# Kernel tuning notes

Measured on AMD Instinct MI355X. Metric: run time of the kernel, lower is better.

The kernel has to match this reference:

```python
import jax, jax.numpy as jnp
import numpy as np

B, S, H = 64, 2048, 1024
X0, X1, X2, A = 1024, 512, 512, 512


def setup_inputs() -> dict:
    key = jax.random.key(0)
    ks = jax.random.split(key, 11)
    wb = np.sqrt(6.0 / (H + A)).astype(np.float32)
    w0b = np.sqrt(6.0 / (X0 + A)).astype(np.float32)
    w1b = np.sqrt(6.0 / (X1 + A)).astype(np.float32)
    w2b = np.sqrt(6.0 / (X2 + A)).astype(np.float32)
    return {
        "hidden_states": jax.random.normal(ks[0], (B, S, H), dtype=jnp.float32),
        "x0_hidden_states": jax.random.normal(ks[1], (B, X0), dtype=jnp.float32),
        "x1_hidden_states": jax.random.normal(ks[2], (B, X1), dtype=jnp.float32),
        "x2_hidden_states": jax.random.normal(ks[3], (B, X2), dtype=jnp.float32),
        "lengths": jax.random.randint(ks[4], (B,), 1, S + 1),
        # torch Linear stores weight as [out, in]
        "Wh_w": jax.random.uniform(ks[5], (A, H), minval=-wb, maxval=wb, dtype=jnp.float32),
        "Wh_b": jnp.zeros((A,), dtype=jnp.float32),
        "W0_w": jax.random.uniform(ks[6], (A, X0), minval=-w0b, maxval=w0b, dtype=jnp.float32),
        "W1_w": jax.random.uniform(ks[7], (A, X1), minval=-w1b, maxval=w1b, dtype=jnp.float32),
        "W2_w": jax.random.uniform(ks[8], (A, X2), minval=-w2b, maxval=w2b, dtype=jnp.float32),
        "V_w": 0.1 * jax.random.normal(ks[9], (1, A), dtype=jnp.float32),
    }


def reference(hidden_states, x0_hidden_states, x1_hidden_states, x2_hidden_states,
              lengths, Wh_w, Wh_b, W0_w, W1_w, W2_w, V_w):
    # Ah: [B,S,A]; context projections broadcast over seq dim
    Ah = jnp.einsum('bsh,ah->bsa', hidden_states, Wh_w) + Wh_b
    A0 = (x0_hidden_states @ W0_w.T)[:, None, :]
    A1 = (x1_hidden_states @ W1_w.T)[:, None, :]
    A2 = (x2_hidden_states @ W2_w.T)[:, None, :]
    w = jax.nn.relu(Ah + A0 + A1 + A2)
    scores = jnp.einsum('bsa,a->bs', w, V_w[0])  # [B,S]
    mask = jnp.arange(scores.shape[1])[None, :] < lengths[:, None]
    scores = jnp.where(mask, scores, -jnp.inf)
    attention_prob = jax.nn.softmax(scores, axis=1)
    output = jnp.einsum('bs,bsh->bh', attention_prob, hidden_states)
    return output, attention_prob
```

## Files before the change

kernel.cpp:

```cpp
#include <hip/hip_runtime.h>
#include <hip/hip_bf16.h>
#include <stdint.h>

#define B_ 64
#define S_ 2048
#define H_ 1024
#define X0_ 1024
#define X1_ 512
#define X2_ 512
#define A_ 512

typedef __attribute__((ext_vector_type(8))) short short8;
typedef __attribute__((ext_vector_type(8))) __bf16 bf16x8;
typedef __attribute__((ext_vector_type(4))) float floatx4;

typedef __attribute__((address_space(1))) const void glb_cv;
typedef __attribute__((address_space(3))) void lds_v;

__device__ inline unsigned short f2bf(float f) {
    union { float f; unsigned u; } v; v.f = f;
    unsigned u = v.u;
    unsigned r = u + 0x7FFF + ((u >> 16) & 1);
    return (unsigned short)(r >> 16);
}

__device__ inline short hwbf(float f) {
    return (short)__builtin_bit_cast(unsigned short, __float2bfloat16(f));
}

__global__ void k_convert_wh(const float* __restrict__ wh, unsigned short* __restrict__ whb) {
    int i = (blockIdx.x * 256 + threadIdx.x) * 4;
    float4 f = *(const float4*)(wh + i);
    ushort4 o;
    o.x = f2bf(f.x); o.y = f2bf(f.y); o.z = f2bf(f.z); o.w = f2bf(f.w);
    *(ushort4*)(whb + i) = o;
}

__global__ void k_ctx(const float* __restrict__ x0, const float* __restrict__ x1,
                      const float* __restrict__ x2, const float* __restrict__ w0,
                      const float* __restrict__ w1, const float* __restrict__ w2,
                      const float* __restrict__ bias, float* __restrict__ ctx) {
    __shared__ float xs[X0_ + X1_ + X2_];
    int b = blockIdx.x >> 4;
    int a0 = (blockIdx.x & 15) << 5;
    int t = threadIdx.x;
    for (int i = t; i < X0_; i += 256) xs[i] = x0[b * X0_ + i];
    for (int i = t; i < X1_; i += 256) xs[X0_ + i] = x1[b * X1_ + i];
    for (int i = t; i < X2_; i += 256) xs[X0_ + X1_ + i] = x2[b * X2_ + i];
    __syncthreads();
    int wave = t >> 6, lane = t & 63;
    for (int j = 0; j < 8; j++) {
        int a = a0 + wave * 8 + j;
        float acc = 0.f;
        const float* r0 = w0 + (size_t)a * X0_;
        for (int k = lane; k < X0_; k += 64) acc += r0[k] * xs[k];
        const float* r1 = w1 + (size_t)a * X1_;
        for (int k = lane; k < X1_; k += 64) acc += r1[k] * xs[X0_ + k];
        const float* r2 = w2 + (size_t)a * X2_;
        for (int k = lane; k < X2_; k += 64) acc += r2[k] * xs[X0_ + X1_ + k];
        for (int off = 32; off; off >>= 1) acc += __shfl_down(acc, off, 64);
        if (lane == 0) ctx[b * A_ + a] = acc + bias[a];
    }
}

__launch_bounds__(256, 2)
__global__ void k_scores(const float* __restrict__ hidden, const unsigned short* __restrict__ whb,
                         const float* __restrict__ ctx, const float* __restrict__ vw,
                         const int* __restrict__ lengths, float* __restrict__ partial) {
    int g = blockIdx.x;
    int xcd = g & 7;
    int i4 = g >> 3;
    int nblk = i4 & 3;
    int grp = xcd * 128 + (i4 >> 2);
    int b = grp >> 4;
    int mt = grp & 15;
    int s0 = mt * 128;
    if (s0 >= lengths[b]) return;
    int n0b = nblk * 128;

    __shared__ unsigned short As[128 * 32];
    __shared__ unsigned short Bs[128 * 32];
    __shared__ float sred[4][64];

    int t = threadIdx.x;
    int wv = t >> 6, lane = t & 63;
    int nl = lane & 15, quad = lane >> 4;
    int wm0 = (wv & 1) * 64;
    int wn0 = (wv >> 1) * 64;

    int c0 = wv * 64 + lane;
    int c1 = c0 + 256;
    const float* abase = hidden + (size_t)(b * S_ + s0) * H_;
    const unsigned short* bbase = whb + (size_t)n0b * H_;
    size_t aoff0 = (size_t)(c0 >> 2) * H_ + (c0 & 3) * 8;
    size_t aoff1 = (size_t)(c1 >> 2) * H_ + (c1 & 3) * 8;

    float4 a0a = *(const float4*)(abase + aoff0);
    float4 a0b = *(const float4*)(abase + aoff0 + 4);
    float4 a1a = *(const float4*)(abase + aoff1);
    float4 a1b = *(const float4*)(abase + aoff1 + 4);

    floatx4 acc[4][4];
#pragma unroll
    for (int i = 0; i < 4; i++)
#pragma unroll
        for (int j = 0; j < 4; j++) acc[i][j] = (floatx4){0.f, 0.f, 0.f, 0.f};

    for (int k0 = 0; k0 < H_; k0 += 32) {
#pragma unroll
        for (int i = 0; i < 2; i++) {
            int c = wv * 64 + i * 256 + lane;
            const unsigned short* gb = bbase + (size_t)(c >> 2) * H_ + k0 + (c & 3) * 8;
            __builtin_amdgcn_global_load_lds((glb_cv*)gb,
                (lds_v*)(Bs + (wv * 64 + i * 256) * 8), 16, 0, 0);
        }
        short8 pa, pb;
        pa[0] = hwbf(a0a.x); pa[1] = hwbf(a0a.y); pa[2] = hwbf(a0a.z); pa[3] = hwbf(a0a.w);
        pa[4] = hwbf(a0b.x); pa[5] = hwbf(a0b.y); pa[6] = hwbf(a0b.z); pa[7] = hwbf(a0b.w);
        pb[0] = hwbf(a1a.x); pb[1] = hwbf(a1a.y); pb[2] = hwbf(a1a.z); pb[3] = hwbf(a1a.w);
        pb[4] = hwbf(a1b.x); pb[5] = hwbf(a1b.y); pb[6] = hwbf(a1b.z); pb[7] = hwbf(a1b.w);
        *(short8*)&As[c0 * 8] = pa;
        *(short8*)&As[c1 * 8] = pb;
        __syncthreads();

        if (k0 + 32 < H_) {
            a0a = *(const float4*)(abase + aoff0 + k0 + 32);
            a0b = *(const float4*)(abase + aoff0 + k0 + 36);
            a1a = *(const float4*)(abase + aoff1 + k0 + 32);
            a1b = *(const float4*)(abase + aoff1 + k0 + 36);
        }

        short8 af[4];
#pragma unroll
        for (int m = 0; m < 4; m++)
            af[m] = *(const short8*)&As[(wm0 + m * 16 + nl) * 32 + quad * 8];
#pragma unroll
        for (int n = 0; n < 4; n++) {
            short8 bfr = *(const short8*)&Bs[(wn0 + n * 16 + nl) * 32 + quad * 8];
            bf16x8 bfv = __builtin_bit_cast(bf16x8, bfr);
#pragma unroll
            for (int m = 0; m < 4; m++) {
                bf16x8 afv = __builtin_bit_cast(bf16x8, af[m]);
                acc[m][n] = __builtin_amdgcn_mfma_f32_16x16x32_bf16(afv, bfv, acc[m][n], 0, 0, 0);
            }
        }
        __syncthreads();
    }

    float cv[4], cc[4];
#pragma unroll
    for (int n = 0; n < 4; n++) {
        int gn = n0b + wn0 + n * 16 + nl;
        cv[n] = vw[gn];
        cc[n] = ctx[b * A_ + gn];
    }
#pragma unroll
    for (int m = 0; m < 4; m++) {
#pragma unroll
        for (int r = 0; r < 4; r++) {
            float sv = 0.f;
#pragma unroll
            for (int n = 0; n < 4; n++) {
                float x = acc[m][n][r] + cc[n];
                sv += (x > 0.f) ? x * cv[n] : 0.f;
            }
#pragma unroll
            for (int off = 1; off < 16; off <<= 1) sv += __shfl_xor(sv, off, 16);
            if (nl == 0) sred[wv][m * 16 + quad * 4 + r] = sv;
        }
    }
    __syncthreads();
    if (t < 128) {
        int h = t >> 6;
        float s = sred[h][t & 63] + sred[h + 2][t & 63];
        partial[((size_t)nblk * B_ + b) * S_ + s0 + t] = s;
    }
}

__global__ void k_softmax(const float* __restrict__ partial, const int* __restrict__ lengths,
                          float* __restrict__ scores, float* __restrict__ probs) {
    int b = blockIdx.x;
    int len = lengths[b];
    int t = threadIdx.x;
    __shared__ float red[256];
    float mx = -1e30f;
    for (int s = t; s < len; s += 256) {
        float sc = partial[(size_t)b * S_ + s] + partial[((size_t)B_ + b) * S_ + s] +
                   partial[((size_t)2 * B_ + b) * S_ + s] + partial[((size_t)3 * B_ + b) * S_ + s];
        scores[b * S_ + s] = sc;
        mx = fmaxf(mx, sc);
    }
    red[t] = mx; __syncthreads();
    for (int off = 128; off; off >>= 1) {
        if (t < off) red[t] = fmaxf(red[t], red[t + off]);
        __syncthreads();
    }
    mx = red[0]; __syncthreads();
    float sum = 0.f;
    for (int s = t; s < len; s += 256) sum += __expf(scores[b * S_ + s] - mx);
    red[t] = sum; __syncthreads();
    for (int off = 128; off; off >>= 1) {
        if (t < off) red[t] += red[t + off];
        __syncthreads();
    }
    float inv = 1.f / red[0];
    for (int s = t; s < S_; s += 256)
        probs[b * S_ + s] = (s < len) ? __expf(scores[b * S_ + s] - mx) * inv : 0.f;
}

__global__ void k_weighted(const float* __restrict__ hidden, const float* __restrict__ probs,
                           const int* __restrict__ lengths, float* __restrict__ partial) {
    int blk = blockIdx.x;
    int b = blk >> 4, ch = blk & 15;
    int len = lengths[b];
    int s0 = ch * 128;
    if (s0 >= len) return;
    int send = min(s0 + 128, len);
    int t = threadIdx.x;
    float4 acc = {0.f, 0.f, 0.f, 0.f};
    const float* hb = hidden + (size_t)(b * S_ + s0) * H_ + t * 4;
    const float* pb = probs + b * S_;
    int s = s0;
    for (; s + 1 < send; s += 2) {
        float p0 = pb[s], p1 = pb[s + 1];
        float4 h0 = *(const float4*)hb;
        float4 h1 = *(const float4*)(hb + H_);
        acc.x += p0 * h0.x + p1 * h1.x;
        acc.y += p0 * h0.y + p1 * h1.y;
        acc.z += p0 * h0.z + p1 * h1.z;
        acc.w += p0 * h0.w + p1 * h1.w;
        hb += 2 * H_;
    }
    if (s < send) {
        float p = pb[s];
        float4 h = *(const float4*)hb;
        acc.x += p * h.x; acc.y += p * h.y; acc.z += p * h.z; acc.w += p * h.w;
    }
    *(float4*)(partial + ((size_t)ch * B_ + b) * H_ + t * 4) = acc;
}

__global__ void k_reduce(const float* __restrict__ partial, const int* __restrict__ lengths,
                         float* __restrict__ out) {
    int i = blockIdx.x * 256 + threadIdx.x;
    int b = i >> 10;
    int h = i & 1023;
    int len = lengths[b];
    int nch = (len + 127) >> 7;
    float s = 0.f;
    for (int c = 0; c < nch; c++) s += partial[((size_t)c * B_ + b) * H_ + h];
    out[i] = s;
}

extern "C" void kernel_launch(void* const* d_in, const int* in_sizes, int n_in,
                              void* d_out, int out_size, void* d_ws, size_t ws_size,
                              hipStream_t stream) {
    const float* hidden = (const float*)d_in[0];
    const float* x0 = (const float*)d_in[1];
    const float* x1 = (const float*)d_in[2];
    const float* x2 = (const float*)d_in[3];
    const int* lengths = (const int*)d_in[4];
    const float* wh_w = (const float*)d_in[5];
    const float* wh_b = (const float*)d_in[6];
    const float* w0_w = (const float*)d_in[7];
    const float* w1_w = (const float*)d_in[8];
    const float* w2_w = (const float*)d_in[9];
    const float* v_w = (const float*)d_in[10];

    float* out = (float*)d_out;
    float* probs = out + B_ * H_;

    char* ws = (char*)d_ws;
    float* ctx = (float*)ws;
    unsigned short* whb = (unsigned short*)(ws + (1 << 17));
    float* scores = (float*)(ws + (1 << 17) + (1 << 20));
    float* pscore = (float*)(ws + (1 << 17) + (1 << 20) + (1 << 19));
    float* pout = (float*)(ws + (1 << 17) + (1 << 20) + (1 << 19) + (1 << 21));

    k_convert_wh<<<dim3(A_ * H_ / 1024), dim3(256), 0, stream>>>(wh_w, whb);
    k_ctx<<<dim3(B_ * (A_ / 32)), dim3(256), 0, stream>>>(x0, x1, x2, w0_w, w1_w, w2_w, wh_b, ctx);
    k_scores<<<dim3(B_ * 64), dim3(256), 0, stream>>>(hidden, whb, ctx, v_w, lengths, pscore);
    k_softmax<<<dim3(B_), dim3(256), 0, stream>>>(pscore, lengths, scores, probs);
    k_weighted<<<dim3(B_ * 16), dim3(256), 0, stream>>>(hidden, probs, lengths, pout);
    k_reduce<<<dim3(B_ * H_ / 256), dim3(256), 0, stream>>>(pout, lengths, out);
}
```

Baseline: 847.0 us.

## Widen score GEMM tile to full attention dim, dropping N-split partials

The scores kernel now uses 512-thread blocks that each compute all 512 attention columns for a 128-row sequence tile, instead of four blocks each covering 128 columns. Each hidden-state tile is therefore read from global memory and converted to bf16 once rather than four times, and the per-column-block partial score buffer disappears, so softmax reads final scores directly. The cost is a larger LDS footprint (32 KB of B tile), twice as many accumulator registers per thread, and a quarter as many blocks, which may lower occupancy and parallelism.

```diff
diff --git a/kernel.cpp b/kernel.cpp
--- a/kernel.cpp
+++ b/kernel.cpp
@@ -63,71 +63,56 @@
     }
 }
 
-__launch_bounds__(256, 2)
+__launch_bounds__(512, 2)
 __global__ void k_scores(const float* __restrict__ hidden, const unsigned short* __restrict__ whb,
                          const float* __restrict__ ctx, const float* __restrict__ vw,
-                         const int* __restrict__ lengths, float* __restrict__ partial) {
+                         const int* __restrict__ lengths, float* __restrict__ scores) {
     int g = blockIdx.x;
-    int xcd = g & 7;
-    int i4 = g >> 3;
-    int nblk = i4 & 3;
-    int grp = xcd * 128 + (i4 >> 2);
+    int grp = (g & 7) * 128 + (g >> 3);
     int b = grp >> 4;
     int mt = grp & 15;
     int s0 = mt * 128;
     if (s0 >= lengths[b]) return;
-    int n0b = nblk * 128;
 
     __shared__ unsigned short As[128 * 32];
-    __shared__ unsigned short Bs[128 * 32];
-    __shared__ float sred[4][64];
+    __shared__ unsigned short Bs[512 * 32];
+    __shared__ float sred[8][64];
 
     int t = threadIdx.x;
     int wv = t >> 6, lane = t & 63;
     int nl = lane & 15, quad = lane >> 4;
     int wm0 = (wv & 1) * 64;
-    int wn0 = (wv >> 1) * 64;
-
-    int c0 = wv * 64 + lane;
-    int c1 = c0 + 256;
+    int wn0 = (wv >> 1) * 128;
+
     const float* abase = hidden + (size_t)(b * S_ + s0) * H_;
-    const unsigned short* bbase = whb + (size_t)n0b * H_;
-    size_t aoff0 = (size_t)(c0 >> 2) * H_ + (c0 & 3) * 8;
-    size_t aoff1 = (size_t)(c1 >> 2) * H_ + (c1 & 3) * 8;
-
-    float4 a0a = *(const float4*)(abase + aoff0);
-    float4 a0b = *(const float4*)(abase + aoff0 + 4);
-    float4 a1a = *(const float4*)(abase + aoff1);
-    float4 a1b = *(const float4*)(abase + aoff1 + 4);
-
-    floatx4 acc[4][4];
+    size_t aoff = (size_t)(t >> 2) * H_ + (t & 3) * 8;
+
+    float4 a0a = *(const float4*)(abase + aoff);
+    float4 a0b = *(const float4*)(abase + aoff + 4);
+
+    floatx4 acc[4][8];
 #pragma unroll
     for (int i = 0; i < 4; i++)
 #pragma unroll
-        for (int j = 0; j < 4; j++) acc[i][j] = (floatx4){0.f, 0.f, 0.f, 0.f};
+        for (int j = 0; j < 8; j++) acc[i][j] = (floatx4){0.f, 0.f, 0.f, 0.f};
 
     for (int k0 = 0; k0 < H_; k0 += 32) {
 #pragma unroll
-        for (int i = 0; i < 2; i++) {
-            int c = wv * 64 + i * 256 + lane;
-            const unsigned short* gb = bbase + (size_t)(c >> 2) * H_ + k0 + (c & 3) * 8;
+        for (int i = 0; i < 4; i++) {
+            int c = wv * 64 + i * 512 + lane;
+            const unsigned short* gb = whb + (size_t)(c >> 2) * H_ + k0 + (c & 3) * 8;
             __builtin_amdgcn_global_load_lds((glb_cv*)gb,
-                (lds_v*)(Bs + (wv * 64 + i * 256) * 8), 16, 0, 0);
-        }
-        short8 pa, pb;
+                (lds_v*)(Bs + (wv * 64 + i * 512) * 8), 16, 0, 0);
+        }
+        short8 pa;
         pa[0] = hwbf(a0a.x); pa[1] = hwbf(a0a.y); pa[2] = hwbf(a0a.z); pa[3] = hwbf(a0a.w);
         pa[4] = hwbf(a0b.x); pa[5] = hwbf(a0b.y); pa[6] = hwbf(a0b.z); pa[7] = hwbf(a0b.w);
-        pb[0] = hwbf(a1a.x); pb[1] = hwbf(a1a.y); pb[2] = hwbf(a1a.z); pb[3] = hwbf(a1a.w);
-        pb[4] = hwbf(a1b.x); pb[5] = hwbf(a1b.y); pb[6] = hwbf(a1b.z); pb[7] = hwbf(a1b.w);
-        *(short8*)&As[c0 * 8] = pa;
-        *(short8*)&As[c1 * 8] = pb;
+        *(short8*)&As[t * 8] = pa;
         __syncthreads();
 
         if (k0 + 32 < H_) {
-            a0a = *(const float4*)(abase + aoff0 + k0 + 32);
-            a0b = *(const float4*)(abase + aoff0 + k0 + 36);
-            a1a = *(const float4*)(abase + aoff1 + k0 + 32);
-            a1b = *(const float4*)(abase + aoff1 + k0 + 36);
+            a0a = *(const float4*)(abase + aoff + k0 + 32);
+            a0b = *(const float4*)(abase + aoff + k0 + 36);
         }
 
         short8 af[4];
@@ -135,7 +120,7 @@
         for (int m = 0; m < 4; m++)
             af[m] = *(const short8*)&As[(wm0 + m * 16 + nl) * 32 + quad * 8];
 #pragma unroll
-        for (int n = 0; n < 4; n++) {
+        for (int n = 0; n < 8; n++) {
             short8 bfr = *(const short8*)&Bs[(wn0 + n * 16 + nl) * 32 + quad * 8];
             bf16x8 bfv = __builtin_bit_cast(bf16x8, bfr);
 #pragma unroll
@@ -147,10 +132,10 @@
         __syncthreads();
     }
 
-    float cv[4], cc[4];
-#pragma unroll
-    for (int n = 0; n < 4; n++) {
-        int gn = n0b + wn0 + n * 16 + nl;
+    float cv[8], cc[8];
+#pragma unroll
+    for (int n = 0; n < 8; n++) {
+        int gn = wn0 + n * 16 + nl;
         cv[n] = vw[gn];
         cc[n] = ctx[b * A_ + gn];
     }
@@ -160,7 +145,7 @@
         for (int r = 0; r < 4; r++) {
             float sv = 0.f;
 #pragma unroll
-            for (int n = 0; n < 4; n++) {
+            for (int n = 0; n < 8; n++) {
                 float x = acc[m][n][r] + cc[n];
                 sv += (x > 0.f) ? x * cv[n] : 0.f;
             }
@@ -171,25 +156,20 @@
     }
     __syncthreads();
     if (t < 128) {
-        int h = t >> 6;
-        float s = sred[h][t & 63] + sred[h + 2][t & 63];
-        partial[((size_t)nblk * B_ + b) * S_ + s0 + t] = s;
-    }
-}
-
-__global__ void k_softmax(const float* __restrict__ partial, const int* __restrict__ lengths,
-                          float* __restrict__ scores, float* __restrict__ probs) {
+        int h = t >> 6, row = t & 63;
+        float s = sred[h][row] + sred[2 + h][row] + sred[4 + h][row] + sred[6 + h][row];
+        scores[(size_t)b * S_ + s0 + t] = s;
+    }
+}
+
+__global__ void k_softmax(const float* __restrict__ scores, const int* __restrict__ lengths,
+                          float* __restrict__ probs) {
     int b = blockIdx.x;
     int len = lengths[b];
     int t = threadIdx.x;
     __shared__ float red[256];
     float mx = -1e30f;
-    for (int s = t; s < len; s += 256) {
-        float sc = partial[(size_t)b * S_ + s] + partial[((size_t)B_ + b) * S_ + s] +
-                   partial[((size_t)2 * B_ + b) * S_ + s] + partial[((size_t)3 * B_ + b) * S_ + s];
-        scores[b * S_ + s] = sc;
-        mx = fmaxf(mx, sc);
-    }
+    for (int s = t; s < len; s += 256) mx = fmaxf(mx, scores[(size_t)b * S_ + s]);
     red[t] = mx; __syncthreads();
     for (int off = 128; off; off >>= 1) {
         if (t < off) red[t] = fmaxf(red[t], red[t + off]);
@@ -197,7 +177,7 @@
     }
     mx = red[0]; __syncthreads();
     float sum = 0.f;
-    for (int s = t; s < len; s += 256) sum += __expf(scores[b * S_ + s] - mx);
+    for (int s = t; s < len; s += 256) sum += __expf(scores[(size_t)b * S_ + s] - mx);
     red[t] = sum; __syncthreads();
     for (int off = 128; off; off >>= 1) {
         if (t < off) red[t] += red[t + off];
@@ -205,7 +185,7 @@
     }
     float inv = 1.f / red[0];
     for (int s = t; s < S_; s += 256)
-        probs[b * S_ + s] = (s < len) ? __expf(scores[b * S_ + s] - mx) * inv : 0.f;
+        probs[b * S_ + s] = (s < len) ? __expf(scores[(size_t)b * S_ + s] - mx) * inv : 0.f;
 }
 
 __global__ void k_weighted(const float* __restrict__ hidden, const float* __restrict__ probs,
@@ -273,13 +253,12 @@
     float* ctx = (float*)ws;
     unsigned short* whb = (unsigned short*)(ws + (1 << 17));
     float* scores = (float*)(ws + (1 << 17) + (1 << 20));
-    float* pscore = (float*)(ws + (1 << 17) + (1 << 20) + (1 << 19));
-    float* pout = (float*)(ws + (1 << 17) + (1 << 20) + (1 << 19) + (1 << 21));
+    float* pout = (float*)(ws + (1 << 17) + (1 << 20) + (1 << 19));
 
     k_convert_wh<<<dim3(A_ * H_ / 1024), dim3(256), 0, stream>>>(wh_w, whb);
     k_ctx<<<dim3(B_ * (A_ / 32)), dim3(256), 0, stream>>>(x0, x1, x2, w0_w, w1_w, w2_w, wh_b, ctx);
-    k_scores<<<dim3(B_ * 64), dim3(256), 0, stream>>>(hidden, whb, ctx, v_w, lengths, pscore);
-    k_softmax<<<dim3(B_), dim3(256), 0, stream>>>(pscore, lengths, scores, probs);
+    k_scores<<<dim3(B_ * 16), dim3(512), 0, stream>>>(hidden, whb, ctx, v_w, lengths, scores);
+    k_softmax<<<dim3(B_), dim3(256), 0, stream>>>(scores, lengths, probs);
     k_weighted<<<dim3(B_ * 16), dim3(256), 0, stream>>>(hidden, probs, lengths, pout);
     k_reduce<<<dim3(B_ * H_ / 256), dim3(256), 0, stream>>>(pout, lengths, out);
 }
```

Measured after the change: 829.7 us. 2.0% less time.
